# Performance work log

Measured on AMD Instinct MI355X. Metric: run time of the kernel, lower is better.

Reference implementation:

```python
import jax, jax.numpy as jnp
import numpy as np

SLIDING_WINDOW = 4
M = 450

def setup_inputs() -> dict:
    P, C, d = 256, 128, 128
    key = jax.random.key(0)
    ks = jax.random.split(key, 16)
    n = lambda k, shape: jax.random.normal(k, shape, dtype=jnp.float32)
    # Linear init scale ~ 1/sqrt(fan_in) to keep activations sane
    s_m = 1.0 / np.sqrt(M)
    return {
        "x": n(ks[0], (8, P, C)),
        "t": 8,
        "TwE": n(ks[1], (SLIDING_WINDOW, d)),
        "PE": n(ks[2], (P, d)),
        "CE": n(ks[3], (C, d)),
        "mE": n(ks[4], (M, d)),
        "ext_W1": n(ks[5], (M, M)) * s_m,
        "ext_b1": n(ks[6], (M,)) * s_m,
        "ext_W2": n(ks[7], (M, M)) * s_m,
        "ext_b2": n(ks[8], (M,)) * s_m,
        "dec_W1": n(ks[9], (M, M)) * s_m,
        "dec_b1": n(ks[10], (M,)) * s_m,
        "dec_W2": n(ks[11], (4 * P * C, M)) * s_m,
        "dec_b2": n(ks[12], (4 * P * C,)) * s_m,
    }

def reference(x, t, TwE, PE, CE, mE, ext_W1, ext_b1, ext_W2, ext_b2,
              dec_W1, dec_b1, dec_W2, dec_b2):
    P, C = PE.shape[0], CE.shape[0]
    xw = x[-SLIDING_WINDOW:]  # (4, P, C)
    # Factorized CP contraction: identical math to
    # einsum('ti,pi,ci,mi->tpcm') followed by einsum('tpcm,tpc->m'),
    # but reduces over t,p,c first without materializing the rank-4 tensor.
    f = jnp.einsum('tpc,ti,pi,ci->i', xw, TwE, PE, CE)  # (d,)
    feat = mE @ f  # (m,)
    # extractor_MLP: Linear(m,m) -> ReLU -> Linear(m,m)
    feat = ext_W2 @ jax.nn.relu(ext_W1 @ feat + ext_b1) + ext_b2
    # dec: Linear(m,m) -> ReLU -> Linear(m, 4*P*C)
    out = dec_W2 @ jax.nn.relu(dec_W1 @ feat + dec_b1) + dec_b2
    return out.reshape(4, P, C)
```

## Files before the change

kernel.cpp:

```cpp
#include <hip/hip_runtime.h>

typedef float vf4 __attribute__((ext_vector_type(4)));

#define WS_F     0
#define WS_FEAT0 128
#define WS_H1    640
#define WS_FEAT  1152
#define WS_H2    1664

__global__ __launch_bounds__(256) void k_f(
    const float* __restrict__ x, const float* __restrict__ TwE,
    const float* __restrict__ PE, const float* __restrict__ CE,
    float* __restrict__ f) {
  const int i = blockIdx.x;
  const int tid = threadIdx.x;
  __shared__ float sCE[128];
  __shared__ float sPE[256];
  __shared__ float sTw[4];
  __shared__ float coef[1024];
  __shared__ float red[4];
  if (tid < 128) sCE[tid] = CE[tid * 128 + i];
  sPE[tid] = PE[tid * 128 + i];
  if (tid < 4) sTw[tid] = TwE[tid * 128 + i];
  __syncthreads();
#pragma unroll
  for (int k = 0; k < 4; ++k) {
    int q = tid + (k << 8);
    coef[q] = sTw[q >> 8] * sPE[q & 255];
  }
  __syncthreads();
  const int lane = tid & 63;
  const int wv = tid >> 6;
  const float2 ce = ((const float2*)sCE)[lane];
  const float2* Xw = (const float2*)(x + 4 * 256 * 128);
  float acc = 0.f;
  const int q0 = wv * 256;
#pragma unroll 8
  for (int k = 0; k < 256; ++k) {
    int q = q0 + k;
    float2 v = Xw[q * 64 + lane];
    acc += coef[q] * (v.x * ce.x + v.y * ce.y);
  }
#pragma unroll
  for (int off = 32; off > 0; off >>= 1) acc += __shfl_down(acc, off);
  if (lane == 0) red[wv] = acc;
  __syncthreads();
  if (tid == 0) f[i] = red[0] + red[1] + red[2] + red[3];
}

__global__ __launch_bounds__(256) void k_mE(
    const float* __restrict__ mE, const float* __restrict__ f,
    float* __restrict__ feat0) {
  __shared__ float sf[128];
  const int tid = threadIdx.x;
  if (tid < 128) sf[tid] = f[tid];
  __syncthreads();
  const int lane = tid & 63;
  const int row = blockIdx.x * 4 + (tid >> 6);
  if (row >= 450) return;
  float2 v = ((const float2*)(mE + row * 128))[lane];
  float acc = v.x * sf[2 * lane] + v.y * sf[2 * lane + 1];
#pragma unroll
  for (int off = 32; off > 0; off >>= 1) acc += __shfl_down(acc, off);
  if (lane == 0) feat0[row] = acc;
}

__global__ __launch_bounds__(256) void k_mv450(
    const float* __restrict__ W, const float* __restrict__ b,
    const float* __restrict__ vin, float* __restrict__ vout, int relu) {
  __shared__ float sv[450];
  const int tid = threadIdx.x;
  if (tid < 450) sv[tid] = vin[tid];
  if (tid + 256 < 450) sv[tid + 256] = vin[tid + 256];
  __syncthreads();
  const int lane = tid & 63;
  const int row = blockIdx.x * 4 + (tid >> 6);
  if (row >= 450) return;
  const float2* Wr = (const float2*)(W + row * 450);
  float acc = 0.f;
#pragma unroll
  for (int k = 0; k < 4; ++k) {
    int idx = lane + (k << 6);
    if (idx < 225) {
      float2 w = Wr[idx];
      acc += w.x * sv[2 * idx] + w.y * sv[2 * idx + 1];
    }
  }
#pragma unroll
  for (int off = 32; off > 0; off >>= 1) acc += __shfl_down(acc, off);
  if (lane == 0) {
    float r = acc + b[row];
    if (relu) r = fmaxf(r, 0.f);
    vout[row] = r;
  }
}

__global__ __launch_bounds__(256) void k_dec2(
    const float* __restrict__ W, const float* __restrict__ b,
    const float* __restrict__ h, float* __restrict__ out) {
  __shared__ float sv2[900];
  const int tid = threadIdx.x;
  for (int k = tid; k < 900; k += 256) sv2[k] = h[k < 450 ? k : k - 450];
  __syncthreads();
  const int lane = tid & 63;
  const int rp = blockIdx.x * 4 + (tid >> 6);
  const vf4* Wp = (const vf4*)(W + (size_t)rp * 900);
  float accA = 0.f, accB = 0.f;
#pragma unroll
  for (int k = 0; k < 3; ++k) {
    int j = lane + (k << 6);
    vf4 w = __builtin_nontemporal_load(&Wp[j]);
    const float* s = &sv2[4 * j];
    float p01 = w.x * s[0] + w.y * s[1];
    float p23 = w.z * s[2] + w.w * s[3];
    if (4 * j + 3 < 450)      accA += p01 + p23;
    else if (4 * j >= 450)    accB += p01 + p23;
    else { accA += p01; accB += p23; }
  }
  if (lane < 33) {
    int j = 192 + lane;
    vf4 w = __builtin_nontemporal_load(&Wp[j]);
    const float* s = &sv2[4 * j];
    accB += w.x * s[0] + w.y * s[1] + w.z * s[2] + w.w * s[3];
  }
#pragma unroll
  for (int off = 32; off > 0; off >>= 1) {
    accA += __shfl_down(accA, off);
    accB += __shfl_down(accB, off);
  }
  if (lane == 0) {
    int r = rp * 2;
    __builtin_nontemporal_store(accA + b[r],     &out[r]);
    __builtin_nontemporal_store(accB + b[r + 1], &out[r + 1]);
  }
}

extern "C" void kernel_launch(void* const* d_in, const int* in_sizes, int n_in,
                              void* d_out, int out_size, void* d_ws, size_t ws_size,
                              hipStream_t stream) {
  const float* x   = (const float*)d_in[0];
  const float* TwE = (const float*)d_in[2];
  const float* PE  = (const float*)d_in[3];
  const float* CE  = (const float*)d_in[4];
  const float* mE  = (const float*)d_in[5];
  const float* eW1 = (const float*)d_in[6];
  const float* eb1 = (const float*)d_in[7];
  const float* eW2 = (const float*)d_in[8];
  const float* eb2 = (const float*)d_in[9];
  const float* dW1 = (const float*)d_in[10];
  const float* db1 = (const float*)d_in[11];
  const float* dW2 = (const float*)d_in[12];
  const float* db2 = (const float*)d_in[13];
  float* out = (float*)d_out;
  float* ws  = (float*)d_ws;

  k_f    <<<128,   256, 0, stream>>>(x, TwE, PE, CE, ws + WS_F);
  k_mE   <<<113,   256, 0, stream>>>(mE, ws + WS_F, ws + WS_FEAT0);
  k_mv450<<<113,   256, 0, stream>>>(eW1, eb1, ws + WS_FEAT0, ws + WS_H1, 1);
  k_mv450<<<113,   256, 0, stream>>>(eW2, eb2, ws + WS_H1, ws + WS_FEAT, 0);
  k_mv450<<<113,   256, 0, stream>>>(dW1, db1, ws + WS_FEAT, ws + WS_H2, 1);
  k_dec2 <<<16384, 256, 0, stream>>>(dW2, db2, ws + WS_H2, out);
}
```

Measured before the change: 374.7 us.

## Split f reduction across two blocks per index and fuse mE matvec into ext layer 1

k_f now launches two blocks per feature index, each covering half of the time window, and writes partial sums. Those partials are added inside a new k_h1 kernel. k_h1 redundantly recomputes the full mE@f product in every block and then performs the first extractor matvec with ReLU, which removes one kernel launch and one global round-trip. The cost is that each of the 113 blocks does a 450x128 matvec from cache, and the loop over mE rows reads with per-thread strided accesses.

```diff
diff --git a/kernel.cpp b/kernel.cpp
--- a/kernel.cpp
+++ b/kernel.cpp
@@ -2,8 +2,7 @@
 
 typedef float vf4 __attribute__((ext_vector_type(4)));
 
-#define WS_F     0
-#define WS_FEAT0 128
+#define WS_FPART 0
 #define WS_H1    640
 #define WS_FEAT  1152
 #define WS_H2    1664
@@ -11,22 +10,23 @@
 __global__ __launch_bounds__(256) void k_f(
     const float* __restrict__ x, const float* __restrict__ TwE,
     const float* __restrict__ PE, const float* __restrict__ CE,
-    float* __restrict__ f) {
-  const int i = blockIdx.x;
+    float* __restrict__ fpart) {
+  const int i   = blockIdx.x >> 1;
+  const int sub = blockIdx.x & 1;
   const int tid = threadIdx.x;
   __shared__ float sCE[128];
   __shared__ float sPE[256];
-  __shared__ float sTw[4];
-  __shared__ float coef[1024];
+  __shared__ float sTw[2];
+  __shared__ float coef[512];
   __shared__ float red[4];
   if (tid < 128) sCE[tid] = CE[tid * 128 + i];
   sPE[tid] = PE[tid * 128 + i];
-  if (tid < 4) sTw[tid] = TwE[tid * 128 + i];
+  if (tid < 2) sTw[tid] = TwE[(sub * 2 + tid) * 128 + i];
   __syncthreads();
 #pragma unroll
-  for (int k = 0; k < 4; ++k) {
-    int q = tid + (k << 8);
-    coef[q] = sTw[q >> 8] * sPE[q & 255];
+  for (int k = 0; k < 2; ++k) {
+    int l = tid + (k << 8);
+    coef[l] = sTw[l >> 8] * sPE[l & 255];
   }
   __syncthreads();
   const int lane = tid & 63;
@@ -34,35 +34,61 @@
   const float2 ce = ((const float2*)sCE)[lane];
   const float2* Xw = (const float2*)(x + 4 * 256 * 128);
   float acc = 0.f;
-  const int q0 = wv * 256;
+  const int l0 = wv * 128;
 #pragma unroll 8
-  for (int k = 0; k < 256; ++k) {
-    int q = q0 + k;
+  for (int k = 0; k < 128; ++k) {
+    int l = l0 + k;
+    int q = (sub << 9) + l;
     float2 v = Xw[q * 64 + lane];
-    acc += coef[q] * (v.x * ce.x + v.y * ce.y);
+    acc += coef[l] * (v.x * ce.x + v.y * ce.y);
   }
 #pragma unroll
   for (int off = 32; off > 0; off >>= 1) acc += __shfl_down(acc, off);
   if (lane == 0) red[wv] = acc;
   __syncthreads();
-  if (tid == 0) f[i] = red[0] + red[1] + red[2] + red[3];
+  if (tid == 0) fpart[sub * 128 + i] = red[0] + red[1] + red[2] + red[3];
 }
 
-__global__ __launch_bounds__(256) void k_mE(
-    const float* __restrict__ mE, const float* __restrict__ f,
-    float* __restrict__ feat0) {
+__global__ __launch_bounds__(256) void k_h1(
+    const float* __restrict__ fpart, const float* __restrict__ mE,
+    const float* __restrict__ eW1, const float* __restrict__ eb1,
+    float* __restrict__ h1) {
   __shared__ float sf[128];
+  __shared__ float sfeat0[450];
   const int tid = threadIdx.x;
-  if (tid < 128) sf[tid] = f[tid];
+  if (tid < 128) sf[tid] = fpart[tid] + fpart[128 + tid];
+  __syncthreads();
+  for (int r = tid; r < 450; r += 256) {
+    const float4* row = (const float4*)(mE + r * 128);
+    float a0 = 0.f, a1 = 0.f, a2 = 0.f, a3 = 0.f;
+#pragma unroll 8
+    for (int k = 0; k < 32; ++k) {
+      float4 m = row[k];
+      a0 += m.x * sf[4 * k];
+      a1 += m.y * sf[4 * k + 1];
+      a2 += m.z * sf[4 * k + 2];
+      a3 += m.w * sf[4 * k + 3];
+    }
+    sfeat0[r] = (a0 + a1) + (a2 + a3);
+  }
   __syncthreads();
   const int lane = tid & 63;
   const int row = blockIdx.x * 4 + (tid >> 6);
-  if (row >= 450) return;
-  float2 v = ((const float2*)(mE + row * 128))[lane];
-  float acc = v.x * sf[2 * lane] + v.y * sf[2 * lane + 1];
+  if (row < 450) {
+    const float2* Wr = (const float2*)(eW1 + row * 450);
+    float acc = 0.f;
 #pragma unroll
-  for (int off = 32; off > 0; off >>= 1) acc += __shfl_down(acc, off);
-  if (lane == 0) feat0[row] = acc;
+    for (int k = 0; k < 4; ++k) {
+      int idx = lane + (k << 6);
+      if (idx < 225) {
+        float2 w = Wr[idx];
+        acc += w.x * sfeat0[2 * idx] + w.y * sfeat0[2 * idx + 1];
+      }
+    }
+#pragma unroll
+    for (int off = 32; off > 0; off >>= 1) acc += __shfl_down(acc, off);
+    if (lane == 0) h1[row] = fmaxf(acc + eb1[row], 0.f);
+  }
 }
 
 __global__ __launch_bounds__(256) void k_mv450(
@@ -154,9 +180,8 @@
   float* out = (float*)d_out;
   float* ws  = (float*)d_ws;
 
-  k_f    <<<128,   256, 0, stream>>>(x, TwE, PE, CE, ws + WS_F);
-  k_mE   <<<113,   256, 0, stream>>>(mE, ws + WS_F, ws + WS_FEAT0);
-  k_mv450<<<113,   256, 0, stream>>>(eW1, eb1, ws + WS_FEAT0, ws + WS_H1, 1);
+  k_f    <<<256,   256, 0, stream>>>(x, TwE, PE, CE, ws + WS_FPART);
+  k_h1   <<<113,   256, 0, stream>>>(ws + WS_FPART, mE, eW1, eb1, ws + WS_H1);
   k_mv450<<<113,   256, 0, stream>>>(eW2, eb2, ws + WS_H1, ws + WS_FEAT, 0);
   k_mv450<<<113,   256, 0, stream>>>(dW1, db1, ws + WS_FEAT, ws + WS_H2, 1);
   k_dec2 <<<16384, 256, 0, stream>>>(dW2, db2, ws + WS_H2, out);
```

Measured after the change: 367.9 us. Within noise of the previous version (-1.8%).
